# Optimization experiments

Measured on AMD Instinct MI355X. Metric: run time of the kernel, lower is better.

Reference implementation:

```python
import jax, jax.numpy as jnp
import numpy as np


def setup_inputs() -> dict:
    key = jax.random.key(0)
    k1, k2 = jax.random.split(key)
    B, S, D = 64, 1024, 768
    batch = jax.random.normal(k1, (B, S, D), dtype=jnp.float32)
    # nn.init.uniform_(proj, -0.05, 0.05)
    proj = jax.random.uniform(k2, (D, D), minval=-0.05, maxval=0.05, dtype=jnp.float32)
    return {"batch": batch, "proj": proj}


def reference(batch, proj):
    """dists[b,i,j] = (h_i - h_j)^T A (h_i - h_j)
    Expanded: h_i^T A h_i + h_j^T A h_j - h_i^T A h_j - h_j^T A h_i.
    Avoids the O(B*S^2*D) diffs tensor of the original.
    """
    # P[b,i,:] = h_i^T A  -> (B, S, D)
    P = jnp.einsum('bid,de->bie', batch, proj)
    # cross[b,i,j] = h_i^T A h_j -> (B, S, S)
    cross = jnp.einsum('bie,bje->bij', P, batch)
    q = jnp.einsum('bii->bi', cross)  # h_i^T A h_i, (B, S)
    dists = q[:, :, None] + q[:, None, :] - cross - jnp.swapaxes(cross, 1, 2)
    return dists
```

## Files before the change

### kernel.cpp

```cpp
#include <hip/hip_runtime.h>

#define GLOBAL_AS __attribute__((address_space(1)))
#define LDS_AS    __attribute__((address_space(3)))

typedef __bf16 bf16_t;
typedef __bf16 bf16x8 __attribute__((ext_vector_type(8)));
typedef __bf16 bf16x4 __attribute__((ext_vector_type(4)));
typedef float  f32x4  __attribute__((ext_vector_type(4)));

#define BATCH 64
#define SEQ   1024
#define DIM   768
#define BS_ROWS (BATCH * SEQ)

__device__ __forceinline__ void gl2lds16(const void* g, void* l) {
    __builtin_amdgcn_global_load_lds((GLOBAL_AS const void*)g, (LDS_AS void*)l, 16, 0, 0);
}

__global__ void k_convert(const float* __restrict__ x, bf16_t* __restrict__ y, int n8) {
    int gid = blockIdx.x * 256 + threadIdx.x;
    if (gid >= n8) return;
    const float4* xp = (const float4*)x;
    float4 a = xp[gid * 2];
    float4 b = xp[gid * 2 + 1];
    bf16x8 v;
    v[0] = (bf16_t)a.x; v[1] = (bf16_t)a.y; v[2] = (bf16_t)a.z; v[3] = (bf16_t)a.w;
    v[4] = (bf16_t)b.x; v[5] = (bf16_t)b.y; v[6] = (bf16_t)b.z; v[7] = (bf16_t)b.w;
    ((bf16x8*)y)[gid] = v;
}

__global__ void k_asym(const float* __restrict__ A, bf16_t* __restrict__ S_, int n) {
    int idx = blockIdx.x * 256 + threadIdx.x;
    if (idx >= n) return;
    int d = idx / DIM;
    int e = idx - d * DIM;
    S_[idx] = (bf16_t)(A[idx] + A[e * DIM + d]);
}


__global__ void k_gemm1(const bf16_t* __restrict__ H, const bf16_t* __restrict__ Ag,
                        bf16_t* __restrict__ M) {
    __shared__ bf16_t Asm[128 * 32];
    __shared__ bf16_t Bsm[128 * 32];
    const int t = threadIdx.x;
    const int row0 = blockIdx.y * 128;
    const int col0 = blockIdx.x * 128;
    const int ln = t & 63, w = t >> 6;
    const int wr = w >> 1, wc = w & 1;
    const int r = ln & 15, qd = ln >> 4;
    const int sseg = qd ^ ((r >> 1) & 3);

    const int srow = t >> 2;
    const int gseg = (t & 3) ^ ((t >> 3) & 3);
    const bf16_t* gA0 = H  + (size_t)(row0 + srow) * DIM + gseg * 8;
    const bf16_t* gA1 = gA0 + (size_t)64 * DIM;
    const bf16_t* gB0 = Ag + (size_t)(col0 + srow) * DIM + gseg * 8;
    const bf16_t* gB1 = gB0 + (size_t)64 * DIM;

    f32x4 acc[4][4] = {};

    for (int k0 = 0; k0 < DIM; k0 += 32) {
        gl2lds16(gA0 + k0, &Asm[t * 8]);
        gl2lds16(gA1 + k0, &Asm[2048 + t * 8]);
        gl2lds16(gB0 + k0, &Bsm[t * 8]);
        gl2lds16(gB1 + k0, &Bsm[2048 + t * 8]);
        __syncthreads();

        bf16x8 af[4], bf[4];
#pragma unroll
        for (int mt = 0; mt < 4; ++mt) {
            int m = wr * 64 + mt * 16 + r;
            af[mt] = *(const bf16x8*)&Asm[m * 32 + sseg * 8];
        }
#pragma unroll
        for (int nt = 0; nt < 4; ++nt) {
            int n = wc * 64 + nt * 16 + r;
            bf[nt] = *(const bf16x8*)&Bsm[n * 32 + sseg * 8];
        }
#pragma unroll
        for (int mt = 0; mt < 4; ++mt)
#pragma unroll
            for (int nt = 0; nt < 4; ++nt)
                acc[mt][nt] = __builtin_amdgcn_mfma_f32_16x16x32_bf16(
                    af[mt], bf[nt], acc[mt][nt], 0, 0, 0);
        __syncthreads();
    }

#pragma unroll
    for (int mt = 0; mt < 4; ++mt) {
#pragma unroll
        for (int rI = 0; rI < 4; ++rI) {
            int row = row0 + wr * 64 + mt * 16 + qd * 4 + rI;
            size_t base = (size_t)row * DIM + col0 + wc * 64;
#pragma unroll
            for (int nt = 0; nt < 4; ++nt)
                M[base + nt * 16 + r] = (bf16_t)acc[mt][nt][rI];
        }
    }
}

__global__ void k_q(const bf16_t* __restrict__ M, const bf16_t* __restrict__ H,
                    float* __restrict__ qv) {
    int t = threadIdx.x;
    int w = t >> 6, ln = t & 63;
    int row = blockIdx.x * 4 + w;
    const bf16_t* mp = M + (size_t)row * DIM;
    const bf16_t* hp = H + (size_t)row * DIM;
    float acc = 0.f;
#pragma unroll
    for (int j = 0; j < 3; ++j) {
        int e = j * 256 + ln * 4;
        bf16x4 mv = *(const bf16x4*)&mp[e];
        bf16x4 hv = *(const bf16x4*)&hp[e];
#pragma unroll
        for (int u = 0; u < 4; ++u) acc += (float)mv[u] * (float)hv[u];
    }
#pragma unroll
    for (int off = 32; off > 0; off >>= 1) acc += __shfl_down(acc, off, 64);
    if (ln == 0) qv[row] = 0.5f * acc;
}

__global__ void k_gemm2(const bf16_t* __restrict__ M, const bf16_t* __restrict__ H,
                        const float* __restrict__ qv, float* __restrict__ out) {
    __shared__ bf16_t Asm[128 * 32];
    __shared__ bf16_t Bsm[128 * 32];
    const int t = threadIdx.x;
    const int b = blockIdx.z;
    const int row0 = blockIdx.y * 128;
    const int col0 = blockIdx.x * 128;
    const int ln = t & 63, w = t >> 6;
    const int wr = w >> 1, wc = w & 1;
    const int r = ln & 15, qd = ln >> 4;
    const int sseg = qd ^ ((r >> 1) & 3);

    const bf16_t* Mb = M + (size_t)b * SEQ * DIM;
    const bf16_t* Hb = H + (size_t)b * SEQ * DIM;

    const int srow = t >> 2;
    const int gseg = (t & 3) ^ ((t >> 3) & 3);
    const bf16_t* gA0 = Mb + (size_t)(row0 + srow) * DIM + gseg * 8;
    const bf16_t* gA1 = gA0 + (size_t)64 * DIM;
    const bf16_t* gB0 = Hb + (size_t)(col0 + srow) * DIM + gseg * 8;
    const bf16_t* gB1 = gB0 + (size_t)64 * DIM;

    f32x4 acc[4][4] = {};

    for (int k0 = 0; k0 < DIM; k0 += 32) {
        gl2lds16(gA0 + k0, &Asm[t * 8]);
        gl2lds16(gA1 + k0, &Asm[2048 + t * 8]);
        gl2lds16(gB0 + k0, &Bsm[t * 8]);
        gl2lds16(gB1 + k0, &Bsm[2048 + t * 8]);
        __syncthreads();

        bf16x8 af[4], bf[4];
#pragma unroll
        for (int mt = 0; mt < 4; ++mt) {
            int m = wr * 64 + mt * 16 + r;
            af[mt] = *(const bf16x8*)&Asm[m * 32 + sseg * 8];
        }
#pragma unroll
        for (int nt = 0; nt < 4; ++nt) {
            int n = wc * 64 + nt * 16 + r;
            bf[nt] = *(const bf16x8*)&Bsm[n * 32 + sseg * 8];
        }
#pragma unroll
        for (int mt = 0; mt < 4; ++mt)
#pragma unroll
            for (int nt = 0; nt < 4; ++nt)
                acc[mt][nt] = __builtin_amdgcn_mfma_f32_16x16x32_bf16(
                    af[mt], bf[nt], acc[mt][nt], 0, 0, 0);
        __syncthreads();
    }

    const float* qb = qv + b * SEQ;
    float qc[4];
#pragma unroll
    for (int nt = 0; nt < 4; ++nt) qc[nt] = qb[col0 + wc * 64 + nt * 16 + r];

#pragma unroll
    for (int mt = 0; mt < 4; ++mt) {
#pragma unroll
        for (int rI = 0; rI < 4; ++rI) {
            int row = row0 + wr * 64 + mt * 16 + qd * 4 + rI;
            float qr = qb[row];
            size_t base = ((size_t)b * SEQ + row) * SEQ + col0 + wc * 64;
#pragma unroll
            for (int nt = 0; nt < 4; ++nt)
                out[base + nt * 16 + r] = qr + qc[nt] - acc[mt][nt][rI];
        }
    }
}

extern "C" void kernel_launch(void* const* d_in, const int* in_sizes, int n_in,
                              void* d_out, int out_size, void* d_ws, size_t ws_size,
                              hipStream_t stream) {
    const float* batch = (const float*)d_in[0];
    const float* proj  = (const float*)d_in[1];
    float* out = (float*)d_out;

    char* ws = (char*)d_ws;
    bf16_t* Hb = (bf16_t*)ws;
    bf16_t* Mb = (bf16_t*)(ws + 100663296);
    bf16_t* Ab = (bf16_t*)(ws + 201326592);
    float*  qv = (float*)(ws + 202506240);

    k_convert<<<24576, 256, 0, stream>>>(batch, Hb, 6291456);
    k_asym<<<2304, 256, 0, stream>>>(proj, Ab, DIM * DIM);
    k_gemm1<<<dim3(DIM / 128, BS_ROWS / 128), 256, 0, stream>>>(Hb, Ab, Mb);
    k_q<<<BS_ROWS / 4, 256, 0, stream>>>(Mb, Hb, qv);
    k_gemm2<<<dim3(SEQ / 128, SEQ / 128, BATCH), 256, 0, stream>>>(Mb, Hb, qv, out);
}
```

Baseline: 697.6 us.

## Exploit output symmetry: compute lower-triangle tiles and mirror-write transposes

The pairwise distance matrix is symmetric because the projection was symmetrized, so the second GEMM now launches only the 36 lower-triangular 128x128 tiles per batch instead of 64. Each off-diagonal tile also writes its transpose using float4 stores along the row dimension. This removes close to half the MFMA and operand-load work of the dominant GEMM, while the output write volume stays the same. The transposed stores are strided across rows, which may coalesce less well.

```diff
diff --git a/kernel.cpp b/kernel.cpp
--- a/kernel.cpp
+++ b/kernel.cpp
@@ -36,7 +36,6 @@
     int e = idx - d * DIM;
     S_[idx] = (bf16_t)(A[idx] + A[e * DIM + d]);
 }
-
 
 __global__ void k_gemm1(const bf16_t* __restrict__ H, const bf16_t* __restrict__ Ag,
                         bf16_t* __restrict__ M) {
@@ -120,14 +119,21 @@
     if (ln == 0) qv[row] = 0.5f * acc;
 }
 
-__global__ void k_gemm2(const bf16_t* __restrict__ M, const bf16_t* __restrict__ H,
-                        const float* __restrict__ qv, float* __restrict__ out) {
+__global__ void k_gemm2_sym(const bf16_t* __restrict__ M, const bf16_t* __restrict__ H,
+                            const float* __restrict__ qv, float* __restrict__ out) {
     __shared__ bf16_t Asm[128 * 32];
     __shared__ bf16_t Bsm[128 * 32];
     const int t = threadIdx.x;
-    const int b = blockIdx.z;
-    const int row0 = blockIdx.y * 128;
-    const int col0 = blockIdx.x * 128;
+    const int b = blockIdx.y;
+
+    int u = blockIdx.x;
+    int ty = (int)((sqrtf(8.f * (float)u + 1.f) - 1.f) * 0.5f);
+    while ((ty + 1) * (ty + 2) / 2 <= u) ++ty;
+    while (ty * (ty + 1) / 2 > u) --ty;
+    const int tx = u - ty * (ty + 1) / 2;
+
+    const int row0 = ty * 128;
+    const int col0 = tx * 128;
     const int ln = t & 63, w = t >> 6;
     const int wr = w >> 1, wc = w & 1;
     const int r = ln & 15, qd = ln >> 4;
@@ -176,17 +182,39 @@
     float qc[4];
 #pragma unroll
     for (int nt = 0; nt < 4; ++nt) qc[nt] = qb[col0 + wc * 64 + nt * 16 + r];
+    float qr[4][4];
+#pragma unroll
+    for (int mt = 0; mt < 4; ++mt)
+#pragma unroll
+        for (int rI = 0; rI < 4; ++rI)
+            qr[mt][rI] = qb[row0 + wr * 64 + mt * 16 + qd * 4 + rI];
 
 #pragma unroll
     for (int mt = 0; mt < 4; ++mt) {
 #pragma unroll
         for (int rI = 0; rI < 4; ++rI) {
             int row = row0 + wr * 64 + mt * 16 + qd * 4 + rI;
-            float qr = qb[row];
             size_t base = ((size_t)b * SEQ + row) * SEQ + col0 + wc * 64;
 #pragma unroll
             for (int nt = 0; nt < 4; ++nt)
-                out[base + nt * 16 + r] = qr + qc[nt] - acc[mt][nt][rI];
+                out[base + nt * 16 + r] = qr[mt][rI] + qc[nt] - acc[mt][nt][rI];
+        }
+    }
+
+    if (ty != tx) {
+#pragma unroll
+        for (int mt = 0; mt < 4; ++mt) {
+            int rowbase = row0 + wr * 64 + mt * 16 + qd * 4;
+#pragma unroll
+            for (int nt = 0; nt < 4; ++nt) {
+                int colg = col0 + wc * 64 + nt * 16 + r;
+                float4 v;
+                v.x = qr[mt][0] + qc[nt] - acc[mt][nt][0];
+                v.y = qr[mt][1] + qc[nt] - acc[mt][nt][1];
+                v.z = qr[mt][2] + qc[nt] - acc[mt][nt][2];
+                v.w = qr[mt][3] + qc[nt] - acc[mt][nt][3];
+                *(float4*)&out[((size_t)b * SEQ + colg) * SEQ + rowbase] = v;
+            }
         }
     }
 }
@@ -208,5 +236,5 @@
     k_asym<<<2304, 256, 0, stream>>>(proj, Ab, DIM * DIM);
     k_gemm1<<<dim3(DIM / 128, BS_ROWS / 128), 256, 0, stream>>>(Hb, Ab, Mb);
     k_q<<<BS_ROWS / 4, 256, 0, stream>>>(Mb, Hb, qv);
-    k_gemm2<<<dim3(SEQ / 128, SEQ / 128, BATCH), 256, 0, stream>>>(Mb, Hb, qv, out);
-}
+    k_gemm2_sym<<<dim3(36, BATCH), 256, 0, stream>>>(Mb, Hb, qv, out);
+}
```

Result: slower. 796.0 us (+14.1%).
